# Performance work log

Hardware: AMD Instinct MI355X
Metric: run time of the kernel (lower is better)

Reference implementation:

```python
import jax, jax.numpy as jnp
import numpy as np

DIM = 1024
HID = 4 * DIM
N_EXPERTS = 8
TOP_K = 2


def setup_inputs() -> dict:
    key = jax.random.key(0)
    ks = jax.random.split(key, 8)
    s = lambda fan_in: 1.0 / np.sqrt(fan_in)
    x = jax.random.normal(ks[0], (2, 2048, DIM), dtype=jnp.float32)
    Wr = jax.random.uniform(ks[1], (DIM, N_EXPERTS), jnp.float32, -s(DIM), s(DIM))
    br = jnp.zeros((N_EXPERTS,), jnp.float32)
    W1 = jax.random.uniform(ks[2], (N_EXPERTS, DIM, HID), jnp.float32, -s(DIM), s(DIM))
    b1 = jnp.zeros((N_EXPERTS, HID), jnp.float32)
    W2 = jax.random.uniform(ks[3], (N_EXPERTS, HID, DIM), jnp.float32, -s(HID), s(HID))
    b2 = jnp.zeros((N_EXPERTS, DIM), jnp.float32)
    return {"x": x, "Wr": Wr, "br": br, "W1": W1, "b1": b1, "W2": W2, "b2": b2}


def reference(x, Wr, br, W1, b1, W2, b2):
    B, S, D = x.shape
    xf = x.reshape(-1, D)                      # [T, D]
    T = xf.shape[0]
    logits = xf @ Wr + br                      # [T, E]
    topw, sel = jax.lax.top_k(logits, TOP_K)   # [T, k]
    topw = jax.nn.softmax(topw, axis=-1)       # softmax over selected experts only
    # dense per-token, per-expert weight (0 for unselected experts)
    w_full = jnp.zeros((T, N_EXPERTS), xf.dtype).at[jnp.arange(T)[:, None], sel].add(topw)
    # run every expert densely (reference baseline), weighted combine
    h = jax.nn.gelu(jnp.einsum('td,edh->teh', xf, W1) + b1, approximate=False)  # [T,E,H]
    y = jnp.einsum('teh,ehd->ted', h, W2) + b2                                   # [T,E,D]
    out = jnp.einsum('ted,te->td', y, w_full)
    return out.reshape(B, S, D)
```

## Files before the change

kernel.cpp:

```cpp
#include <hip/hip_runtime.h>
#include <math.h>

#define DIM 1024
#define HID 4096
#define NE 8
#define NTOK 4096

typedef short s16x8 __attribute__((ext_vector_type(8)));
typedef float f32x4 __attribute__((ext_vector_type(4)));

__device__ __forceinline__ unsigned short f2bf(float f) {
  unsigned int u = __float_as_uint(f);
  u = u + 0x7fffu + ((u >> 16) & 1u);
  return (unsigned short)(u >> 16);
}

__device__ __forceinline__ void gll16(const void* g, void* l) {
  __builtin_amdgcn_global_load_lds(
      (const __attribute__((address_space(1))) unsigned int*)g,
      (__attribute__((address_space(3))) unsigned int*)l, 16, 0, 0);
}

__global__ __launch_bounds__(256) void zero_k(float4* out4, int* ctrl) {
  int i = blockIdx.x * 256 + threadIdx.x;
  out4[i] = make_float4(0.f, 0.f, 0.f, 0.f);
  if (i < 32) ctrl[i] = 0;
}

__global__ __launch_bounds__(256) void router_k(const float* __restrict__ x,
    const float* __restrict__ Wr, const float* __restrict__ br,
    short* __restrict__ xbf, int* __restrict__ ctrl,
    int* __restrict__ sel, float* __restrict__ selw) {
  __shared__ float lred[4 * NE];
  int t = blockIdx.x, tid = threadIdx.x;
  const float* xr = x + (size_t)t * DIM;
  float p[NE];
#pragma unroll
  for (int e = 0; e < NE; ++e) p[e] = 0.f;
#pragma unroll
  for (int it = 0; it < DIM / 256; ++it) {
    int d = it * 256 + tid;
    float xv = xr[d];
    xbf[(size_t)t * DIM + d] = (short)f2bf(xv);
#pragma unroll
    for (int e = 0; e < NE; ++e) p[e] += xv * Wr[d * NE + e];
  }
#pragma unroll
  for (int e = 0; e < NE; ++e) {
    float v = p[e];
#pragma unroll
    for (int off = 32; off > 0; off >>= 1) v += __shfl_down(v, off);
    if ((tid & 63) == 0) lred[(tid >> 6) * NE + e] = v;
  }
  __syncthreads();
  if (tid == 0) {
    float lg[NE];
#pragma unroll
    for (int e = 0; e < NE; ++e)
      lg[e] = lred[e] + lred[NE + e] + lred[2 * NE + e] + lred[3 * NE + e] + br[e];
    int b0 = 0; float v0 = lg[0];
    for (int e = 1; e < NE; ++e) if (lg[e] > v0) { v0 = lg[e]; b0 = e; }
    int b1i = -1; float v1 = -3.4e38f;
    for (int e = 0; e < NE; ++e) if (e != b0 && lg[e] > v1) { v1 = lg[e]; b1i = e; }
    float e1 = expf(v1 - v0);
    float inv = 1.f / (1.f + e1);
    sel[t * 2] = b0; sel[t * 2 + 1] = b1i;
    selw[t * 2] = inv; selw[t * 2 + 1] = e1 * inv;
    atomicAdd(&ctrl[b0], 1); atomicAdd(&ctrl[b1i], 1);
  }
}

__global__ void scan_k(int* ctrl) {
  if (threadIdx.x == 0) {
    int o = 0;
#pragma unroll
    for (int e = 0; e < NE; ++e) { ctrl[8 + e] = o; o += ctrl[e]; }
    ctrl[16] = o;
  }
}

__global__ __launch_bounds__(256) void build_k(const int* __restrict__ sel,
    const float* __restrict__ selw, int* ctrl,
    int* __restrict__ slot_tok, float* __restrict__ slot_w) {
  int t = blockIdx.x * 256 + threadIdx.x;
  if (t >= NTOK) return;
#pragma unroll
  for (int k = 0; k < 2; ++k) {
    int e = sel[t * 2 + k];
    int pos = atomicAdd(&ctrl[20 + e], 1);
    int s = ctrl[8 + e] + pos;
    slot_tok[s] = t;
    slot_w[s] = selw[t * 2 + k];
  }
}

__global__ __launch_bounds__(256) void gemm1_k(const short* __restrict__ xbf,
    const float* __restrict__ W1, const float* __restrict__ b1,
    const int* __restrict__ ctrl, const int* __restrict__ slot_tok,
    short* __restrict__ h) {
  int e = blockIdx.z, my = blockIdx.y, bx = blockIdx.x;
  int cnt = ctrl[e];
  if (my * 128 >= cnt) return;
  int slot0 = ctrl[8 + e];
  int tid = threadIdx.x, lane = tid & 63;
  int wv = tid >> 6, wm = wv >> 1, wn = wv & 1;
  __shared__ __attribute__((aligned(16))) short ldsA[128 * 32];
  __shared__ __attribute__((aligned(16))) short ldsB[128 * 40];

  const short* ap[2]; short* la[2];
#pragma unroll
  for (int i = 0; i < 2; ++i) {
    int c = tid + i * 256;
    int row = c >> 2;
    int srow = min(my * 128 + row, cnt - 1);
    int tok = slot_tok[slot0 + srow];
    ap[i] = xbf + (size_t)tok * DIM + (c & 3) * 8;
    la[i] = &ldsA[c * 8];
  }
  int n0 = (tid & 63) * 2;
  int kg = tid >> 6;
  const float* bp = W1 + ((size_t)e * DIM + kg * 8) * HID + bx * 128 + n0;
  short* lb0 = &ldsB[(n0) * 40 + kg * 8];
  short* lb1 = &ldsB[(n0 + 1) * 40 + kg * 8];

  f32x4 acc[4][4];
#pragma unroll
  for (int i = 0; i < 4; ++i)
#pragma unroll
    for (int j = 0; j < 4; ++j) acc[i][j] = (f32x4){0.f, 0.f, 0.f, 0.f};

#pragma unroll 2
  for (int kt = 0; kt < DIM / 32; ++kt) {
    float2 fv[8];
#pragma unroll
    for (int kk = 0; kk < 8; ++kk)
      fv[kk] = *(const float2*)&bp[(size_t)kk * HID];
    __syncthreads();
    gll16(ap[0], la[0]);
    gll16(ap[1], la[1]);
    s16x8 v0, v1;
#pragma unroll
    for (int kk = 0; kk < 8; ++kk) {
      v0[kk] = (short)f2bf(fv[kk].x);
      v1[kk] = (short)f2bf(fv[kk].y);
    }
    *(s16x8*)lb0 = v0;
    *(s16x8*)lb1 = v1;
    asm volatile("s_waitcnt vmcnt(0)" ::: "memory");
    __syncthreads();
    s16x8 aF[4], bF[4];
#pragma unroll
    for (int i = 0; i < 4; ++i)
      aF[i] = *(const s16x8*)&ldsA[(wm * 64 + i * 16 + (lane & 15)) * 32 + (lane >> 4) * 8];
#pragma unroll
    for (int j = 0; j < 4; ++j)
      bF[j] = *(const s16x8*)&ldsB[(wn * 64 + j * 16 + (lane & 15)) * 40 + (lane >> 4) * 8];
#pragma unroll
    for (int i = 0; i < 4; ++i)
#pragma unroll
      for (int j = 0; j < 4; ++j)
        acc[i][j] = __builtin_amdgcn_mfma_f32_16x16x32_bf16(aF[i], bF[j], acc[i][j], 0, 0, 0);
    ap[0] += 32; ap[1] += 32; bp += (size_t)32 * HID;
  }
#pragma unroll
  for (int i = 0; i < 4; ++i) {
#pragma unroll
    for (int r = 0; r < 4; ++r) {
      int row_l = wm * 64 + i * 16 + (lane >> 4) * 4 + r;
      int grow = my * 128 + row_l;
      if (grow < cnt) {
#pragma unroll
        for (int j = 0; j < 4; ++j) {
          int col = bx * 128 + wn * 64 + j * 16 + (lane & 15);
          float z = acc[i][j][r] + b1[e * HID + col];
          float g = 0.5f * z * (1.f + erff(z * 0.70710678118f));
          h[(size_t)(slot0 + grow) * HID + col] = (short)f2bf(g);
        }
      }
    }
  }
}

__global__ __launch_bounds__(256) void gemm2_k(const short* __restrict__ h,
    const float* __restrict__ W2, const float* __restrict__ b2,
    const int* __restrict__ ctrl, const int* __restrict__ slot_tok,
    const float* __restrict__ slot_w, float* __restrict__ out) {
  int e = blockIdx.z, my = blockIdx.y, bx = blockIdx.x;
  int cnt = ctrl[e];
  if (my * 128 >= cnt) return;
  int slot0 = ctrl[8 + e];
  int tid = threadIdx.x, lane = tid & 63;
  int wv = tid >> 6, wm = wv >> 1, wn = wv & 1;
  __shared__ __attribute__((aligned(16))) short ldsA[128 * 32];
  __shared__ __attribute__((aligned(16))) short ldsB[128 * 40];
  __shared__ int stok[128];
  __shared__ float swt[128];
  if (tid < 128) {
    int srow = min(my * 128 + tid, cnt - 1);
    stok[tid] = slot_tok[slot0 + srow];
    swt[tid] = slot_w[slot0 + srow];
  }
  const short* ap[2]; short* la[2];
#pragma unroll
  for (int i = 0; i < 2; ++i) {
    int c = tid + i * 256;
    int row = c >> 2;
    int srow = min(my * 128 + row, cnt - 1);
    ap[i] = h + (size_t)(slot0 + srow) * HID + (c & 3) * 8;
    la[i] = &ldsA[c * 8];
  }
  int n0 = (tid & 63) * 2;
  int kg = tid >> 6;
  const float* bp = W2 + ((size_t)e * HID + kg * 8) * DIM + bx * 128 + n0;
  short* lb0 = &ldsB[(n0) * 40 + kg * 8];
  short* lb1 = &ldsB[(n0 + 1) * 40 + kg * 8];

  f32x4 acc[4][4];
#pragma unroll
  for (int i = 0; i < 4; ++i)
#pragma unroll
    for (int j = 0; j < 4; ++j) acc[i][j] = (f32x4){0.f, 0.f, 0.f, 0.f};

#pragma unroll 2
  for (int kt = 0; kt < HID / 32; ++kt) {
    float2 fv[8];
#pragma unroll
    for (int kk = 0; kk < 8; ++kk)
      fv[kk] = *(const float2*)&bp[(size_t)kk * DIM];
    __syncthreads();
    gll16(ap[0], la[0]);
    gll16(ap[1], la[1]);
    s16x8 v0, v1;
#pragma unroll
    for (int kk = 0; kk < 8; ++kk) {
      v0[kk] = (short)f2bf(fv[kk].x);
      v1[kk] = (short)f2bf(fv[kk].y);
    }
    *(s16x8*)lb0 = v0;
    *(s16x8*)lb1 = v1;
    asm volatile("s_waitcnt vmcnt(0)" ::: "memory");
    __syncthreads();
    s16x8 aF[4], bF[4];
#pragma unroll
    for (int i = 0; i < 4; ++i)
      aF[i] = *(const s16x8*)&ldsA[(wm * 64 + i * 16 + (lane & 15)) * 32 + (lane >> 4) * 8];
#pragma unroll
    for (int j = 0; j < 4; ++j)
      bF[j] = *(const s16x8*)&ldsB[(wn * 64 + j * 16 + (lane & 15)) * 40 + (lane >> 4) * 8];
#pragma unroll
    for (int i = 0; i < 4; ++i)
#pragma unroll
      for (int j = 0; j < 4; ++j)
        acc[i][j] = __builtin_amdgcn_mfma_f32_16x16x32_bf16(aF[i], bF[j], acc[i][j], 0, 0, 0);
    ap[0] += 32; ap[1] += 32; bp += (size_t)32 * DIM;
  }
#pragma unroll
  for (int i = 0; i < 4; ++i) {
#pragma unroll
    for (int r = 0; r < 4; ++r) {
      int row_l = wm * 64 + i * 16 + (lane >> 4) * 4 + r;
      int grow = my * 128 + row_l;
      if (grow < cnt) {
        int tok = stok[row_l];
        float wrow = swt[row_l];
#pragma unroll
        for (int j = 0; j < 4; ++j) {
          int col = bx * 128 + wn * 64 + j * 16 + (lane & 15);
          float y = acc[i][j][r] + b2[e * DIM + col];
          unsafeAtomicAdd(&out[(size_t)tok * DIM + col], wrow * y);
        }
      }
    }
  }
}

extern "C" void kernel_launch(void* const* d_in, const int* in_sizes, int n_in,
                              void* d_out, int out_size, void* d_ws, size_t ws_size,
                              hipStream_t stream) {
  const float* x  = (const float*)d_in[0];
  const float* Wr = (const float*)d_in[1];
  const float* br = (const float*)d_in[2];
  const float* W1 = (const float*)d_in[3];
  const float* b1 = (const float*)d_in[4];
  const float* W2 = (const float*)d_in[5];
  const float* b2 = (const float*)d_in[6];
  float* out = (float*)d_out;

  char* ws = (char*)d_ws;
  int*   ctrl     = (int*)(ws);
  int*   sel      = (int*)(ws + 1024);
  float* selw     = (float*)(ws + 33792);
  int*   slot_tok = (int*)(ws + 66560);
  float* slot_w   = (float*)(ws + 99328);
  short* xbf      = (short*)(ws + (1u << 20));
  short* h        = (short*)(ws + (16u << 20));

  zero_k<<<(NTOK * DIM / 4) / 256, 256, 0, stream>>>((float4*)out, ctrl);
  router_k<<<NTOK, 256, 0, stream>>>(x, Wr, br, xbf, ctrl, sel, selw);
  scan_k<<<1, 64, 0, stream>>>(ctrl);
  build_k<<<NTOK / 256, 256, 0, stream>>>(sel, selw, ctrl, slot_tok, slot_w);
  gemm1_k<<<dim3(HID / 128, NTOK / 128, NE), 256, 0, stream>>>(xbf, W1, b1, ctrl, slot_tok, h);
  gemm2_k<<<dim3(DIM / 128, NTOK / 128, NE), 256, 0, stream>>>(h, W2, b2, ctrl, slot_tok, slot_w, out);
}
```

Measured before the change: 826.6 us.

## Pre-transpose expert weights to bf16 and use double-buffered swizzled GEMMs with split-K

Adds a per-call kernel that converts W1 and W2 from fp32 to bf16 and transposes them into a K-contiguous layout in workspace. New GEMM kernels then load both operands with direct global-to-LDS copies into double-buffered, XOR-swizzled shared memory, so the next tile is fetched while MFMAs run on the current one. The second GEMM also splits K four ways to raise grid parallelism, at the cost of more atomic adds to the output. The path is taken only when the workspace is large enough, and the extra conversion pass adds memory traffic on every call.

Result: no change. 841.3 us (+1.8%).

```diff
diff --git a/kernel.cpp b/kernel.cpp
--- a/kernel.cpp
+++ b/kernel.cpp
@@ -91,6 +91,203 @@
     int s = ctrl[8 + e] + pos;
     slot_tok[s] = t;
     slot_w[s] = selw[t * 2 + k];
+  }
+}
+
+__global__ __launch_bounds__(256) void tcvt_k(const float* __restrict__ src,
+    short* __restrict__ dst, int K, int N) {
+  __shared__ __attribute__((aligned(16))) short t[64][72];
+  int e = blockIdx.z;
+  int n0 = blockIdx.x * 64, k0 = blockIdx.y * 64;
+  const float* s = src + (size_t)e * K * N;
+  short* d = dst + (size_t)e * N * K;
+  int tid = threadIdx.x;
+#pragma unroll
+  for (int i = 0; i < 4; ++i) {
+    int c = tid + i * 256;
+    int row = c >> 4, c4 = c & 15;
+    float4 v = *(const float4*)&s[(size_t)(k0 + row) * N + n0 + c4 * 4];
+    t[c4 * 4 + 0][row] = (short)f2bf(v.x);
+    t[c4 * 4 + 1][row] = (short)f2bf(v.y);
+    t[c4 * 4 + 2][row] = (short)f2bf(v.z);
+    t[c4 * 4 + 3][row] = (short)f2bf(v.w);
+  }
+  __syncthreads();
+#pragma unroll
+  for (int i = 0; i < 2; ++i) {
+    int c = tid + i * 256;
+    int n = c >> 3, k8 = c & 7;
+    *(s16x8*)&d[(size_t)(n0 + n) * K + k0 + k8 * 8] = *(const s16x8*)&t[n][k8 * 8];
+  }
+}
+
+__global__ __launch_bounds__(256) void gemm1n_k(const short* __restrict__ xbf,
+    const short* __restrict__ w1t, const float* __restrict__ b1,
+    const int* __restrict__ ctrl, const int* __restrict__ slot_tok,
+    short* __restrict__ h) {
+  int e = blockIdx.z, my = blockIdx.y, bx = blockIdx.x;
+  int cnt = ctrl[e];
+  if (my * 128 >= cnt) return;
+  int slot0 = ctrl[8 + e];
+  int tid = threadIdx.x, lane = tid & 63;
+  int wv = tid >> 6, wm = wv >> 1, wn = wv & 1;
+  __shared__ __attribute__((aligned(16))) short ldsA[2][128 * 32];
+  __shared__ __attribute__((aligned(16))) short ldsB[2][128 * 32];
+
+  const short* ga[2]; const short* gb[2]; int lo[2];
+#pragma unroll
+  for (int i = 0; i < 2; ++i) {
+    int c = tid + i * 256;
+    int row = c >> 2;
+    int cs = (c & 3) ^ (row & 3);
+    int srow = min(my * 128 + row, cnt - 1);
+    ga[i] = xbf + (size_t)slot_tok[slot0 + srow] * DIM + cs * 8;
+    gb[i] = w1t + ((size_t)e * HID + bx * 128 + row) * DIM + cs * 8;
+    lo[i] = c * 8;
+  }
+  int koff = ((lane >> 4) ^ (lane & 3)) * 8;
+
+  f32x4 acc[4][4];
+#pragma unroll
+  for (int i = 0; i < 4; ++i)
+#pragma unroll
+    for (int j = 0; j < 4; ++j) acc[i][j] = (f32x4){0.f, 0.f, 0.f, 0.f};
+
+#pragma unroll
+  for (int i = 0; i < 2; ++i) { gll16(ga[i], &ldsA[0][lo[i]]); gll16(gb[i], &ldsB[0][lo[i]]); }
+  __syncthreads();
+
+  const int NT = DIM / 32;
+  for (int t = 0; t < NT; ++t) {
+    int buf = t & 1;
+    if (t + 1 < NT) {
+      int nb = buf ^ 1;
+#pragma unroll
+      for (int i = 0; i < 2; ++i) {
+        gll16(ga[i] + (t + 1) * 32, &ldsA[nb][lo[i]]);
+        gll16(gb[i] + (t + 1) * 32, &ldsB[nb][lo[i]]);
+      }
+    }
+    s16x8 aF[4], bF[4];
+#pragma unroll
+    for (int i = 0; i < 4; ++i)
+      aF[i] = *(const s16x8*)&ldsA[buf][(wm * 64 + i * 16 + (lane & 15)) * 32 + koff];
+#pragma unroll
+    for (int j = 0; j < 4; ++j)
+      bF[j] = *(const s16x8*)&ldsB[buf][(wn * 64 + j * 16 + (lane & 15)) * 32 + koff];
+#pragma unroll
+    for (int i = 0; i < 4; ++i)
+#pragma unroll
+      for (int j = 0; j < 4; ++j)
+        acc[i][j] = __builtin_amdgcn_mfma_f32_16x16x32_bf16(aF[i], bF[j], acc[i][j], 0, 0, 0);
+    __syncthreads();
+  }
+#pragma unroll
+  for (int i = 0; i < 4; ++i) {
+#pragma unroll
+    for (int r = 0; r < 4; ++r) {
+      int row_l = wm * 64 + i * 16 + (lane >> 4) * 4 + r;
+      int grow = my * 128 + row_l;
+      if (grow < cnt) {
+#pragma unroll
+        for (int j = 0; j < 4; ++j) {
+          int col = bx * 128 + wn * 64 + j * 16 + (lane & 15);
+          float z = acc[i][j][r] + b1[e * HID + col];
+          float g = 0.5f * z * (1.f + erff(z * 0.70710678118f));
+          h[(size_t)(slot0 + grow) * HID + col] = (short)f2bf(g);
+        }
+      }
+    }
+  }
+}
+
+__global__ __launch_bounds__(256) void gemm2n_k(const short* __restrict__ h,
+    const short* __restrict__ w2t, const float* __restrict__ b2,
+    const int* __restrict__ ctrl, const int* __restrict__ slot_tok,
+    const float* __restrict__ slot_w, float* __restrict__ out) {
+  int e = blockIdx.z, my = blockIdx.y;
+  int nx = blockIdx.x & 7, kc = blockIdx.x >> 3;
+  int cnt = ctrl[e];
+  if (my * 128 >= cnt) return;
+  int slot0 = ctrl[8 + e];
+  int tid = threadIdx.x, lane = tid & 63;
+  int wv = tid >> 6, wm = wv >> 1, wn = wv & 1;
+  __shared__ __attribute__((aligned(16))) short ldsA[2][128 * 32];
+  __shared__ __attribute__((aligned(16))) short ldsB[2][128 * 32];
+  __shared__ int stok[128];
+  __shared__ float swt[128];
+  if (tid < 128) {
+    int srow = min(my * 128 + tid, cnt - 1);
+    stok[tid] = slot_tok[slot0 + srow];
+    swt[tid] = slot_w[slot0 + srow];
+  }
+  int k0 = kc * (HID / 4);
+  const short* ga[2]; const short* gb[2]; int lo[2];
+#pragma unroll
+  for (int i = 0; i < 2; ++i) {
+    int c = tid + i * 256;
+    int row = c >> 2;
+    int cs = (c & 3) ^ (row & 3);
+    int srow = min(my * 128 + row, cnt - 1);
+    ga[i] = h + (size_t)(slot0 + srow) * HID + k0 + cs * 8;
+    gb[i] = w2t + ((size_t)e * DIM + nx * 128 + row) * HID + k0 + cs * 8;
+    lo[i] = c * 8;
+  }
+  int koff = ((lane >> 4) ^ (lane & 3)) * 8;
+
+  f32x4 acc[4][4];
+#pragma unroll
+  for (int i = 0; i < 4; ++i)
+#pragma unroll
+    for (int j = 0; j < 4; ++j) acc[i][j] = (f32x4){0.f, 0.f, 0.f, 0.f};
+
+#pragma unroll
+  for (int i = 0; i < 2; ++i) { gll16(ga[i], &ldsA[0][lo[i]]); gll16(gb[i], &ldsB[0][lo[i]]); }
+  __syncthreads();
+
+  const int NT = (HID / 4) / 32;
+  for (int t = 0; t < NT; ++t) {
+    int buf = t & 1;
+    if (t + 1 < NT) {
+      int nb = buf ^ 1;
+#pragma unroll
+      for (int i = 0; i < 2; ++i) {
+        gll16(ga[i] + (t + 1) * 32, &ldsA[nb][lo[i]]);
+        gll16(gb[i] + (t + 1) * 32, &ldsB[nb][lo[i]]);
+      }
+    }
+    s16x8 aF[4], bF[4];
+#pragma unroll
+    for (int i = 0; i < 4; ++i)
+      aF[i] = *(const s16x8*)&ldsA[buf][(wm * 64 + i * 16 + (lane & 15)) * 32 + koff];
+#pragma unroll
+    for (int j = 0; j < 4; ++j)
+      bF[j] = *(const s16x8*)&ldsB[buf][(wn * 64 + j * 16 + (lane & 15)) * 32 + koff];
+#pragma unroll
+    for (int i = 0; i < 4; ++i)
+#pragma unroll
+      for (int j = 0; j < 4; ++j)
+        acc[i][j] = __builtin_amdgcn_mfma_f32_16x16x32_bf16(aF[i], bF[j], acc[i][j], 0, 0, 0);
+    __syncthreads();
+  }
+#pragma unroll
+  for (int i = 0; i < 4; ++i) {
+#pragma unroll
+    for (int r = 0; r < 4; ++r) {
+      int row_l = wm * 64 + i * 16 + (lane >> 4) * 4 + r;
+      int grow = my * 128 + row_l;
+      if (grow < cnt) {
+        int tok = stok[row_l];
+        float wrow = swt[row_l];
+#pragma unroll
+        for (int j = 0; j < 4; ++j) {
+          int col = nx * 128 + wn * 64 + j * 16 + (lane & 15);
+          float y = acc[i][j][r];
+          if (kc == 0) y += b2[e * DIM + col];
+          unsafeAtomicAdd(&out[(size_t)tok * DIM + col], wrow * y);
+        }
+      }
+    }
   }
 }
 
@@ -106,7 +303,6 @@
   int wv = tid >> 6, wm = wv >> 1, wn = wv & 1;
   __shared__ __attribute__((aligned(16))) short ldsA[128 * 32];
   __shared__ __attribute__((aligned(16))) short ldsB[128 * 40];
-
   const short* ap[2]; short* la[2];
 #pragma unroll
   for (int i = 0; i < 2; ++i) {
@@ -122,30 +318,22 @@
   const float* bp = W1 + ((size_t)e * DIM + kg * 8) * HID + bx * 128 + n0;
   short* lb0 = &ldsB[(n0) * 40 + kg * 8];
   short* lb1 = &ldsB[(n0 + 1) * 40 + kg * 8];
-
   f32x4 acc[4][4];
 #pragma unroll
   for (int i = 0; i < 4; ++i)
 #pragma unroll
     for (int j = 0; j < 4; ++j) acc[i][j] = (f32x4){0.f, 0.f, 0.f, 0.f};
-
 #pragma unroll 2
   for (int kt = 0; kt < DIM / 32; ++kt) {
     float2 fv[8];
 #pragma unroll
-    for (int kk = 0; kk < 8; ++kk)
-      fv[kk] = *(const float2*)&bp[(size_t)kk * HID];
-    __syncthreads();
-    gll16(ap[0], la[0]);
-    gll16(ap[1], la[1]);
+    for (int kk = 0; kk < 8; ++kk) fv[kk] = *(const float2*)&bp[(size_t)kk * HID];
+    __syncthreads();
+    gll16(ap[0], la[0]); gll16(ap[1], la[1]);
     s16x8 v0, v1;
 #pragma unroll
-    for (int kk = 0; kk < 8; ++kk) {
-      v0[kk] = (short)f2bf(fv[kk].x);
-      v1[kk] = (short)f2bf(fv[kk].y);
-    }
-    *(s16x8*)lb0 = v0;
-    *(s16x8*)lb1 = v1;
+    for (int kk = 0; kk < 8; ++kk) { v0[kk] = (short)f2bf(fv[kk].x); v1[kk] = (short)f2bf(fv[kk].y); }
+    *(s16x8*)lb0 = v0; *(s16x8*)lb1 = v1;
     asm volatile("s_waitcnt vmcnt(0)" ::: "memory");
     __syncthreads();
     s16x8 aF[4], bF[4];
@@ -163,12 +351,12 @@
     ap[0] += 32; ap[1] += 32; bp += (size_t)32 * HID;
   }
 #pragma unroll
-  for (int i = 0; i < 4; ++i) {
+  for (int i = 0; i < 4; ++i)
 #pragma unroll
     for (int r = 0; r < 4; ++r) {
       int row_l = wm * 64 + i * 16 + (lane >> 4) * 4 + r;
       int grow = my * 128 + row_l;
-      if (grow < cnt) {
+      if (grow < cnt)
 #pragma unroll
         for (int j = 0; j < 4; ++j) {
           int col = bx * 128 + wn * 64 + j * 16 + (lane & 15);
@@ -176,9 +364,7 @@
           float g = 0.5f * z * (1.f + erff(z * 0.70710678118f));
           h[(size_t)(slot0 + grow) * HID + col] = (short)f2bf(g);
         }
-      }
-    }
-  }
+    }
 }
 
 __global__ __launch_bounds__(256) void gemm2_k(const short* __restrict__ h,
@@ -214,30 +400,22 @@
   const float* bp = W2 + ((size_t)e * HID + kg * 8) * DIM + bx * 128 + n0;
   short* lb0 = &ldsB[(n0) * 40 + kg * 8];
   short* lb1 = &ldsB[(n0 + 1) * 40 + kg * 8];
-
   f32x4 acc[4][4];
 #pragma unroll
   for (int i = 0; i < 4; ++i)
 #pragma unroll
     for (int j = 0; j < 4; ++j) acc[i][j] = (f32x4){0.f, 0.f, 0.f, 0.f};
-
 #pragma unroll 2
   for (int kt = 0; kt < HID / 32; ++kt) {
     float2 fv[8];
 #pragma unroll
-    for (int kk = 0; kk < 8; ++kk)
-      fv[kk] = *(const float2*)&bp[(size_t)kk * DIM];
-    __syncthreads();
-    gll16(ap[0], la[0]);
-    gll16(ap[1], la[1]);
+    for (int kk = 0; kk < 8; ++kk) fv[kk] = *(const float2*)&bp[(size_t)kk * DIM];
+    __syncthreads();
+    gll16(ap[0], la[0]); gll16(ap[1], la[1]);
     s16x8 v0, v1;
 #pragma unroll
-    for (int kk = 0; kk < 8; ++kk) {
-      v0[kk] = (short)f2bf(fv[kk].x);
-      v1[kk] = (short)f2bf(fv[kk].y);
-    }
-    *(s16x8*)lb0 = v0;
-    *(s16x8*)lb1 = v1;
+    for (int kk = 0; kk < 8; ++kk) { v0[kk] = (short)f2bf(fv[kk].x); v1[kk] = (short)f2bf(fv[kk].y); }
+    *(s16x8*)lb0 = v0; *(s16x8*)lb1 = v1;
     asm volatile("s_waitcnt vmcnt(0)" ::: "memory");
     __syncthreads();
     s16x8 aF[4], bF[4];
@@ -255,7 +433,7 @@
     ap[0] += 32; ap[1] += 32; bp += (size_t)32 * DIM;
   }
 #pragma unroll
-  for (int i = 0; i < 4; ++i) {
+  for (int i = 0; i < 4; ++i)
 #pragma unroll
     for (int r = 0; r < 4; ++r) {
       int row_l = wm * 64 + i * 16 + (lane >> 4) * 4 + r;
@@ -271,7 +449,6 @@
         }
       }
     }
-  }
 }
 
 extern "C" void kernel_launch(void* const* d_in, const int* in_sizes, int n_in,
@@ -287,18 +464,29 @@
   float* out = (float*)d_out;
 
   char* ws = (char*)d_ws;
+  const size_t MiB = 1024 * 1024;
   int*   ctrl     = (int*)(ws);
   int*   sel      = (int*)(ws + 1024);
   float* selw     = (float*)(ws + 33792);
   int*   slot_tok = (int*)(ws + 66560);
   float* slot_w   = (float*)(ws + 99328);
-  short* xbf      = (short*)(ws + (1u << 20));
-  short* h        = (short*)(ws + (16u << 20));
+  short* xbf      = (short*)(ws + 1 * MiB);
+  short* h        = (short*)(ws + 16 * MiB);
+  short* w1t      = (short*)(ws + 80 * MiB);
+  short* w2t      = (short*)(ws + 144 * MiB);
+  bool fat = ws_size >= 208 * MiB;
 
   zero_k<<<(NTOK * DIM / 4) / 256, 256, 0, stream>>>((float4*)out, ctrl);
   router_k<<<NTOK, 256, 0, stream>>>(x, Wr, br, xbf, ctrl, sel, selw);
   scan_k<<<1, 64, 0, stream>>>(ctrl);
   build_k<<<NTOK / 256, 256, 0, stream>>>(sel, selw, ctrl, slot_tok, slot_w);
-  gemm1_k<<<dim3(HID / 128, NTOK / 128, NE), 256, 0, stream>>>(xbf, W1, b1, ctrl, slot_tok, h);
-  gemm2_k<<<dim3(DIM / 128, NTOK / 128, NE), 256, 0, stream>>>(h, W2, b2, ctrl, slot_tok, slot_w, out);
-}
+  if (fat) {
+    tcvt_k<<<dim3(HID / 64, DIM / 64, NE), 256, 0, stream>>>(W1, w1t, DIM, HID);
+    tcvt_k<<<dim3(DIM / 64, HID / 64, NE), 256, 0, stream>>>(W2, w2t, HID, DIM);
+    gemm1n_k<<<dim3(HID / 128, NTOK / 128, NE), 256, 0, stream>>>(xbf, w1t, b1, ctrl, slot_tok, h);
+    gemm2n_k<<<dim3((DIM / 128) * 4, NTOK / 128, NE), 256, 0, stream>>>(h, w2t, b2, ctrl, slot_tok, slot_w, out);
+  } else {
+    gemm1_k<<<dim3(HID / 128, NTOK / 128, NE), 256, 0, stream>>>(xbf, W1, b1, ctrl, slot_tok, h);
+    gemm2_k<<<dim3(DIM / 128, NTOK / 128, NE), 256, 0, stream>>>(h, W2, b2, ctrl, slot_tok, slot_w, out);
+  }
+}
```
